# Optimization experiments

Hardware: AMD Instinct MI355X
Metric: run time of the kernel (lower is better)

## Reference

```python
import jax, jax.numpy as jnp
import numpy as np

N_HEADS = 71
HEAD_DIM = 64
ROPE_BASE = 10000.0
SCALE = 1.0 / np.sqrt(HEAD_DIM)  # 0.125


def setup_inputs() -> dict:
    key = jax.random.key(0)
    k1, k2, k3 = jax.random.split(key, 3)
    B, S, H = 1, 1024, N_HEADS * HEAD_DIM  # 4544
    F = (N_HEADS + 2) * HEAD_DIM           # 4672 fused QKV out features
    hidden_states = jax.random.normal(k1, (B, 1, S, H), dtype=jnp.float32)
    qkv_weight = jax.random.normal(k2, (H, F), dtype=jnp.float32) * 0.02
    dense_weight = jax.random.normal(k3, (H, H), dtype=jnp.float32) * 0.02
    # additive causal mask [1,1,S,S]
    causal = np.tril(np.ones((S, S), dtype=bool))
    attention_mask = jnp.asarray(np.where(causal, 0.0, -1e9).astype(np.float32))[None, None]
    return {"hidden_states": hidden_states, "qkv_weight": qkv_weight,
            "dense_weight": dense_weight, "attention_mask": attention_mask}


def _rope_tables(seq_len):
    inv_freq = 1.0 / (ROPE_BASE ** (jnp.arange(0, HEAD_DIM, 2, dtype=jnp.float32) / HEAD_DIM))
    t = jnp.arange(seq_len, dtype=jnp.float32)
    freqs = t[:, None] * inv_freq[None, :]          # [S, 32]
    emb = jnp.concatenate([freqs, freqs], axis=-1)  # [S, 64]
    return jnp.cos(emb), jnp.sin(emb)


def _rotate_half(x):
    h = HEAD_DIM // 2
    return jnp.concatenate([-x[..., h:], x[..., :h]], axis=-1)


def reference(hidden_states, qkv_weight, dense_weight, attention_mask):
    # Prefill: hidden_states [B, 1, S, H]
    B, _, S, H = hidden_states.shape
    x = hidden_states[:, 0]                                  # [B, S, H]
    qkv = jnp.einsum('bsh,hf->bsf', x, qkv_weight)           # fused QKV matmul
    qd = N_HEADS * HEAD_DIM
    # Falcon-7B MQA head split: 71 query heads, 1 shared K and V head
    q = qkv[..., :qd].reshape(B, S, N_HEADS, HEAD_DIM).transpose(0, 2, 1, 3)  # [B, nH, S, d]
    k = qkv[..., qd:qd + HEAD_DIM]                           # [B, S, d]
    v = qkv[..., qd + HEAD_DIM:]                             # [B, S, d]
    cos, sin = _rope_tables(S)                               # [S, d]
    q = q * cos + _rotate_half(q) * sin
    k = k * cos + _rotate_half(k) * sin
    scores = jnp.einsum('bhqd,bkd->bhqk', q, k) * SCALE      # [B, nH, S, S]
    scores = scores + attention_mask                         # causal mask (alibi is None for Falcon-7B)
    probs = jax.nn.softmax(scores, axis=-1)
    ctx = jnp.einsum('bhqk,bkd->bhqd', probs, v)             # [B, nH, S, d]
    merged = ctx.transpose(0, 2, 1, 3).reshape(B, S, H)      # concat heads
    out = jnp.einsum('bsh,hf->bsf', merged, dense_weight)    # selfout dense
    return out[:, None]                                      # [B, 1, S, H]
```

## Files before the change

kernel.cpp:

```cpp
#include <hip/hip_runtime.h>
#include <hip/hip_bf16.h>

#define DI __device__ __forceinline__

typedef __attribute__((ext_vector_type(8))) short bf16x8;
typedef __attribute__((ext_vector_type(4))) float f32x4;
typedef __attribute__((ext_vector_type(4))) short s16x4;

constexpr int S  = 1024;
constexpr int NH = 71;
constexpr int HD = 64;
constexpr int H  = NH * HD;
constexpr int F  = (NH + 2) * HD;
constexpr float K2 = 0.125f * 1.44269504f;

DI short f2bf(float f) {
  union { float f; unsigned u; } v; v.f = f;
  unsigned r = v.u + 0x7fffu + ((v.u >> 16) & 1u);
  return (short)(r >> 16);
}
DI unsigned cvt_pk_bf16(float lo, float hi) {
  unsigned r;
  asm("v_cvt_pk_bf16_f32 %0, %1, %2" : "=v"(r) : "v"(lo), "v"(hi));
  return r;
}
DI float redmax_g(float x) {
  float y = fmaxf(x, __int_as_float(__builtin_amdgcn_ds_swizzle(__float_as_int(x), 0x401F)));
  return fmaxf(y, __shfl_xor(y, 32));
}
DI float redsum_g(float x) {
  float y = x + __int_as_float(__builtin_amdgcn_ds_swizzle(__float_as_int(x), 0x401F));
  return y + __shfl_xor(y, 32);
}

DI void gload_lds16(const void* g, void* l) {
  __builtin_amdgcn_global_load_lds(
      (const __attribute__((address_space(1))) unsigned int*)g,
      (__attribute__((address_space(3))) unsigned int*)l, 16, 0, 0);
}

DI bf16x8 ldswz(const char* base, int row, int slot) {
  return *(const bf16x8*)(base + row * 128 + ((slot ^ (row & 7)) << 4));
}

__global__ void cast_x_kernel(const float* __restrict__ x, short* __restrict__ xb, int n4) {
  int i = blockIdx.x * blockDim.x + threadIdx.x;
  if (i >= n4) return;
  f32x4 v = ((const f32x4*)x)[i];
  s16x4 o = { f2bf(v.x), f2bf(v.y), f2bf(v.z), f2bf(v.w) };
  ((s16x4*)xb)[i] = o;
}

__global__ __launch_bounds__(256) void transpose_cast_kernel(
    const float* __restrict__ W, short* __restrict__ Wt, int K, int N) {
  __shared__ float tile[64][65];
  int n0 = blockIdx.x * 64, k0 = blockIdx.y * 64;
  int c = threadIdx.x & 63, rg = threadIdx.x >> 6;
#pragma unroll
  for (int i = 0; i < 16; ++i) {
    int r = rg * 16 + i;
    tile[r][c] = W[(size_t)(k0 + r) * N + n0 + c];
  }
  __syncthreads();
#pragma unroll
  for (int i = 0; i < 16; ++i) {
    int r = rg * 16 + i;
    Wt[(size_t)(n0 + r) * K + k0 + c] = f2bf(tile[c][r]);
  }
}

__global__ void rope_tables_kernel(float* __restrict__ ct, float* __restrict__ st) {
  int s = blockIdx.x, i = threadIdx.x;
  float invf = powf(10000.0f, -(float)i / 32.0f);
  float a = (float)s * invf;
  ct[s * 32 + i] = cosf(a);
  st[s * 32 + i] = sinf(a);
}

__global__ __launch_bounds__(256) void rope_pack_kernel(
    const float* __restrict__ qkv, const float* __restrict__ ct, const float* __restrict__ st,
    short* __restrict__ Qb, short* __restrict__ Kb, short* __restrict__ Vt) {
  int s = blockIdx.x;
  const float* row = qkv + (size_t)s * F;
  for (int c = threadIdx.x; c < F; c += 256) {
    int hh = c >> 6, d = c & 63;
    float v = row[c];
    if (hh <= NH) {
      int i = d & 31;
      float cs = ct[s * 32 + i], sn = st[s * 32 + i];
      float rot = (d < 32) ? -row[c + 32] : row[c - 32];
      short ob = f2bf(v * cs + rot * sn);
      if (hh < NH) Qb[((size_t)hh * S + s) * 64 + d] = ob;
      else         Kb[(size_t)s * 64 + d] = ob;
    } else {
      Vt[(size_t)d * S + s] = f2bf(v);
    }
  }
}

__global__ __launch_bounds__(256, 3) void gemm_bt_kernel(
    const short* __restrict__ A, const short* __restrict__ Bt, float* __restrict__ C,
    int M, int N, int K) {
  __shared__ short As[2 * 128 * 64];
  __shared__ short Bs[2 * 64 * 64];
  const int tid = threadIdx.x;
  const int lane = tid & 63;
  const int wave = tid >> 6;
  const int wr = wave >> 1, wc = wave & 1;
  const int lr = lane & 15, g = lane >> 4;

  const int nwg = gridDim.x;
  int bid = blockIdx.x;
  int wgid = ((nwg & 7) == 0) ? ((bid & 7) * (nwg >> 3) + (bid >> 3)) : bid;
  const int ntm = M >> 7;
  const int tn = wgid / ntm;
  const int tm = wgid % ntm;

  f32x4 acc[4][2] = {};

  int srowA[4], skofA[4];
#pragma unroll
  for (int iss = 0; iss < 4; ++iss) {
    int d = iss * 256 + wave * 64 + lane;
    int row = (d >> 2) & 127;
    int c = (d & 3) ^ ((row >> 1) & 3);
    srowA[iss] = row;
    skofA[iss] = ((d >> 9) << 5) + c * 8;
  }
  int srowB[2], skofB[2];
#pragma unroll
  for (int iss = 0; iss < 2; ++iss) {
    int d = iss * 256 + wave * 64 + lane;
    int row = (d >> 2) & 63;
    int c = (d & 3) ^ ((row >> 1) & 3);
    srowB[iss] = row;
    skofB[iss] = ((d >> 8) << 5) + c * 8;
  }
  int offA[2][4], offB[2][2];
#pragma unroll
  for (int im = 0; im < 4; ++im) {
    int row_a = wr * 64 + im * 16 + lr;
    int sl = (g ^ ((row_a >> 1) & 3)) << 4;
#pragma unroll
    for (int kk = 0; kk < 2; ++kk) offA[kk][im] = kk * 8192 + row_a * 64 + sl;
  }
#pragma unroll
  for (int in = 0; in < 2; ++in) {
    int row_b = wc * 32 + in * 16 + lr;
    int sl = (g ^ ((row_b >> 1) & 3)) << 4;
#pragma unroll
    for (int kk = 0; kk < 2; ++kk) offB[kk][in] = kk * 4096 + row_b * 64 + sl;
  }

  char* AsB = (char*)As;
  char* BsB = (char*)Bs;
  const size_t Abase = (size_t)tm * 128 * K;
  const size_t Bbase = (size_t)tn * 64 * K;

#define STAGE(buf, k0)                                                                  \
  {                                                                                     \
    _Pragma("unroll")                                                                   \
    for (int iss = 0; iss < 4; ++iss)                                                   \
      gload_lds16(A + Abase + (size_t)srowA[iss] * K + (k0) + skofA[iss],               \
                  AsB + (buf) * 16384 + (iss * 4 + wave) * 1024);                       \
    _Pragma("unroll")                                                                   \
    for (int iss = 0; iss < 2; ++iss)                                                   \
      gload_lds16(Bt + Bbase + (size_t)srowB[iss] * K + (k0) + skofB[iss],              \
                  BsB + (buf) * 8192 + (iss * 4 + wave) * 1024);                        \
  }

  STAGE(0, 0);
  STAGE(1, 64);
  const int KS = K >> 6;
  for (int t = 0; t < KS; ++t) {
    const int cur = t & 1;
    if (t + 1 < KS) asm volatile("s_waitcnt vmcnt(6)" ::: "memory");
    else            asm volatile("s_waitcnt vmcnt(0)" ::: "memory");
    __builtin_amdgcn_sched_barrier(0);
    __builtin_amdgcn_s_barrier();
    __builtin_amdgcn_sched_barrier(0);
    const char* Ac = AsB + cur * 16384;
    const char* Bc = BsB + cur * 8192;
    bf16x8 af[2][4], bfr[2][2];
#pragma unroll
    for (int kk = 0; kk < 2; ++kk) {
#pragma unroll
      for (int im = 0; im < 4; ++im) af[kk][im] = *(const bf16x8*)(Ac + offA[kk][im]);
#pragma unroll
      for (int in = 0; in < 2; ++in) bfr[kk][in] = *(const bf16x8*)(Bc + offB[kk][in]);
    }
#pragma unroll
    for (int kk = 0; kk < 2; ++kk)
#pragma unroll
      for (int im = 0; im < 4; ++im)
#pragma unroll
        for (int in = 0; in < 2; ++in)
          acc[im][in] = __builtin_amdgcn_mfma_f32_16x16x32_bf16(af[kk][im], bfr[kk][in], acc[im][in], 0, 0, 0);
    __builtin_amdgcn_sched_barrier(0);
    __builtin_amdgcn_s_barrier();
    __builtin_amdgcn_sched_barrier(0);
    if (t + 2 < KS) STAGE(cur, (t + 2) << 6);
  }
#undef STAGE

#pragma unroll
  for (int im = 0; im < 4; ++im) {
#pragma unroll
    for (int in = 0; in < 2; ++in) {
      int row = tm * 128 + wr * 64 + im * 16 + g * 4;
      int col = tn * 64 + wc * 32 + in * 16 + lr;
#pragma unroll
      for (int i = 0; i < 4; ++i)
        C[(size_t)(row + i) * N + col] = acc[im][in][i];
    }
  }
}

DI void attn_step(const char* Kc, const char* Vc, char* P,
                  int key0, int qrow, bf16x8 aQ0, bf16x8 aQ1,
                  f32x4* accO, float& m, float& l, int lr, int g) {
  f32x4 p[4];
#pragma unroll
  for (int nf = 0; nf < 4; ++nf) {
    int row = nf * 16 + lr;
    bf16x8 k0 = ldswz(Kc, row, g);
    bf16x8 k1 = ldswz(Kc, row, g + 4);
    f32x4 z = {};
    z = __builtin_amdgcn_mfma_f32_16x16x32_bf16(k0, aQ0, z, 0, 0, 0);
    p[nf] = __builtin_amdgcn_mfma_f32_16x16x32_bf16(k1, aQ1, z, 0, 0, 0);
  }
  float pmx = -3e30f;
#pragma unroll
  for (int nf = 0; nf < 4; ++nf)
#pragma unroll
    for (int i = 0; i < 4; ++i) {
      int key = key0 + nf * 16 + 4 * g + i;
      float sv = p[nf][i] * K2 + (key <= qrow ? 0.0f : -1e30f);
      p[nf][i] = sv;
      pmx = fmaxf(pmx, sv);
    }
  float pm = redmax_g(pmx);
  float mn = fmaxf(m, pm);
  float scl = __builtin_exp2f(m - mn);
  m = mn;
  float rsx = 0.f;
#pragma unroll
  for (int nf = 0; nf < 4; ++nf) {
    f32x4 pe;
#pragma unroll
    for (int i = 0; i < 4; ++i) {
      pe[i] = __builtin_exp2f(p[nf][i] - m);
      rsx += pe[i];
    }
    uint2 wv;
    wv.x = cvt_pk_bf16(pe[0], pe[1]);
    wv.y = cvt_pk_bf16(pe[2], pe[3]);
    *(uint2*)(P + lr * 144 + nf * 32 + g * 8) = wv;
  }
  float rs = redsum_g(rsx);
  l = l * scl + rs;
#pragma unroll
  for (int df = 0; df < 4; ++df)
#pragma unroll
    for (int i = 0; i < 4; ++i)
      accO[df][i] *= scl;
#pragma unroll
  for (int st = 0; st < 2; ++st) {
    bf16x8 bP = *(const bf16x8*)(P + lr * 144 + st * 64 + g * 16);
#pragma unroll
    for (int df = 0; df < 4; ++df) {
      bf16x8 aV = ldswz(Vc, df * 16 + lr, g + 4 * st);
      accO[df] = __builtin_amdgcn_mfma_f32_16x16x32_bf16(aV, bP, accO[df], 0, 0, 0);
    }
  }
}

__global__ __launch_bounds__(256) void attn_kernel(
    const short* __restrict__ Qb,
    const short* __restrict__ Kb,
    const short* __restrict__ Vt,
    short* __restrict__ merged) {
  __shared__ short Ks[2][4096];
  __shared__ short Vs[2][4096];
  __shared__ short Ps[4][16 * 72];
  const int lane = threadIdx.x & 63, w = threadIdx.x >> 6;
  const int lr = lane & 15, g = lane >> 4;
  const int j = blockIdx.x, head = blockIdx.y;
  const int kbmax = 15 - j;
  const int qA = j * 64 + w * 16 + lr;
  const int qB = (15 - j) * 64 + w * 16 + lr;
  char* KsB = (char*)Ks;
  char* VsB = (char*)Vs;
  char* P = (char*)Ps[w];

  int crow[2], cslot[2];
#pragma unroll
  for (int i = 0; i < 2; ++i) {
    int c = (i * 4 + w) * 64 + lane;
    crow[i] = c >> 3;
    cslot[i] = (c & 7) ^ (crow[i] & 7);
  }

  const short* qap = Qb + ((size_t)head * S + qA) * 64 + g * 8;
  bf16x8 aQA0 = *(const bf16x8*)(qap);
  bf16x8 aQA1 = *(const bf16x8*)(qap + 32);
  const short* qbp = Qb + ((size_t)head * S + qB) * 64 + g * 8;
  bf16x8 aQB0 = *(const bf16x8*)(qbp);
  bf16x8 aQB1 = *(const bf16x8*)(qbp + 32);

  f32x4 accA[4] = {}, accB[4] = {};
  float mA = -3e30f, lA = 0.f, mB = -3e30f, lB = 0.f;

#define STAGEKV(buf, key0)                                                       \
  {                                                                              \
    _Pragma("unroll")                                                            \
    for (int i = 0; i < 2; ++i) {                                                \
      gload_lds16(Kb + (size_t)((key0) + crow[i]) * 64 + cslot[i] * 8,           \
                  KsB + (buf) * 8192 + (i * 4 + w) * 1024);                      \
      gload_lds16(Vt + (size_t)crow[i] * S + (key0) + cslot[i] * 8,              \
                  VsB + (buf) * 8192 + (i * 4 + w) * 1024);                      \
    }                                                                            \
  }

  STAGEKV(0, 0);
  for (int kb = 0; kb <= kbmax; ++kb) {
    const int cur = kb & 1;
    __syncthreads();
    if (kb < kbmax) STAGEKV(cur ^ 1, (kb + 1) * 64);
    const char* Kc = KsB + cur * 8192;
    const char* Vc = VsB + cur * 8192;
    attn_step(Kc, Vc, P, kb * 64, qB, aQB0, aQB1, accB, mB, lB, lr, g);
    if (kb <= j)
      attn_step(Kc, Vc, P, kb * 64, qA, aQA0, aQA1, accA, mA, lA, lr, g);
  }
#undef STAGEKV

  float rlA = 1.0f / lA, rlB = 1.0f / lB;
#pragma unroll
  for (int df = 0; df < 4; ++df)
#pragma unroll
    for (int i = 0; i < 4; ++i) {
      int d = head * 64 + df * 16 + 4 * g + i;
      merged[(size_t)qB * H + d] = f2bf(accB[df][i] * rlB);
      merged[(size_t)qA * H + d] = f2bf(accA[df][i] * rlA);
    }
}

extern "C" void kernel_launch(void* const* d_in, const int* in_sizes, int n_in,
                              void* d_out, int out_size, void* d_ws, size_t ws_size,
                              hipStream_t stream) {
  const float* x    = (const float*)d_in[0];
  const float* wqkv = (const float*)d_in[1];
  const float* wd   = (const float*)d_in[2];
  float* out = (float*)d_out;

  char* ws = (char*)d_ws;
  size_t off = 0;
  short* Wqkvt  = (short*)(ws + off); off += (size_t)F * H * 2;
  short* Wdt    = (short*)(ws + off); off += (size_t)H * H * 2;
  short* Qb     = (short*)(ws + off); off += (size_t)NH * S * HD * 2;
  short* Kb     = (short*)(ws + off); off += (size_t)S * HD * 2;
  short* Vtb    = (short*)(ws + off); off += (size_t)HD * S * 2;
  short* merged = (short*)(ws + off); off += (size_t)S * H * 2;
  float* ct     = (float*)(ws + off); off += (size_t)S * 32 * 4;
  float* st     = (float*)(ws + off); off += (size_t)S * 32 * 4;
  short* xb     = (short*)(ws + off); off += (size_t)S * H * 2;
  float* qkv    = (float*)(ws + off); off += (size_t)S * F * 4;
  (void)ws_size; (void)in_sizes; (void)n_in; (void)out_size;

  hipLaunchKernelGGL(cast_x_kernel, dim3((S * H / 4 + 255) / 256), dim3(256), 0, stream,
                     x, xb, S * H / 4);
  hipLaunchKernelGGL(transpose_cast_kernel, dim3(F / 64, H / 64), dim3(256), 0, stream,
                     wqkv, Wqkvt, H, F);
  hipLaunchKernelGGL(transpose_cast_kernel, dim3(H / 64, H / 64), dim3(256), 0, stream,
                     wd, Wdt, H, H);
  hipLaunchKernelGGL(rope_tables_kernel, dim3(S), dim3(32), 0, stream, ct, st);
  hipLaunchKernelGGL(gemm_bt_kernel, dim3((F / 64) * (S / 128)), dim3(256), 0, stream,
                     xb, Wqkvt, qkv, S, F, H);
  hipLaunchKernelGGL(rope_pack_kernel, dim3(S), dim3(256), 0, stream,
                     qkv, ct, st, Qb, Kb, Vtb);
  hipLaunchKernelGGL(attn_kernel, dim3(8, NH), dim3(256), 0, stream,
                     Qb, Kb, Vtb, merged);
  hipLaunchKernelGGL(gemm_bt_kernel, dim3((H / 64) * (S / 128)), dim3(256), 0, stream,
                     merged, Wdt, out, S, H, H);
}
```

Measured before the change: 244.1 us.

## Replace tiled GEMM with stream-K persistent GEMM using atomic partial accumulation

Both projection GEMMs now use a persistent stream-K kernel with 256 workgroups of 512 threads and 128x128 tiles. The K-iteration space is split evenly across workgroups, and partial tiles are merged into the output with float atomicAdd. This targets wave-quantization imbalance from the ragged tile counts (73 or 71 N tiles by 8 M tiles). In exchange the outputs must be zeroed first by extra kernels, atomics add memory traffic, and the summation order becomes nondeterministic. The kernel also raises MFMA priority with setprio.

New measurement: 324.4 us. 32.9% more time.

```diff
diff --git a/kernel.cpp b/kernel.cpp
--- a/kernel.cpp
+++ b/kernel.cpp
@@ -41,6 +41,13 @@
 
 DI bf16x8 ldswz(const char* base, int row, int slot) {
   return *(const bf16x8*)(base + row * 128 + ((slot ^ (row & 7)) << 4));
+}
+
+__global__ void zero_kernel(float* __restrict__ p, int n4) {
+  int i = blockIdx.x * blockDim.x + threadIdx.x;
+  if (i >= n4) return;
+  f32x4 z = {0.f, 0.f, 0.f, 0.f};
+  ((f32x4*)p)[i] = z;
 }
 
 __global__ void cast_x_kernel(const float* __restrict__ x, short* __restrict__ xb, int n4) {
@@ -98,121 +105,128 @@
   }
 }
 
-__global__ __launch_bounds__(256, 3) void gemm_bt_kernel(
+__global__ __launch_bounds__(512, 2) void gemm_streamk_kernel(
     const short* __restrict__ A, const short* __restrict__ Bt, float* __restrict__ C,
-    int M, int N, int K) {
-  __shared__ short As[2 * 128 * 64];
-  __shared__ short Bs[2 * 64 * 64];
+    int N, int K, int U) {
+  __shared__ f32x4 smemv[4096];
+  char* smem = (char*)smemv;
   const int tid = threadIdx.x;
-  const int lane = tid & 63;
-  const int wave = tid >> 6;
-  const int wr = wave >> 1, wc = wave & 1;
+  const int lane = tid & 63, wave = tid >> 6;
+  const int wr = wave >> 2, wc = wave & 3;
   const int lr = lane & 15, g = lane >> 4;
-
-  const int nwg = gridDim.x;
-  int bid = blockIdx.x;
-  int wgid = ((nwg & 7) == 0) ? ((bid & 7) * (nwg >> 3) + (bid >> 3)) : bid;
-  const int ntm = M >> 7;
-  const int tn = wgid / ntm;
-  const int tm = wgid % ntm;
-
-  f32x4 acc[4][2] = {};
-
-  int srowA[4], skofA[4];
-#pragma unroll
-  for (int iss = 0; iss < 4; ++iss) {
-    int d = iss * 256 + wave * 64 + lane;
+  const int nk = K >> 6;
+
+  const int bid = blockIdx.x;
+  const int swz = ((bid & 7) << 5) | (bid >> 3);
+  const int q = U >> 8, r = U & 255;
+  const int start = swz * q + (swz < r ? swz : r);
+  const int end = start + q + (swz < r ? 1 : 0);
+
+  int rowS[2], kofS[2];
+#pragma unroll
+  for (int iss = 0; iss < 2; ++iss) {
+    int d = iss * 512 + tid;
     int row = (d >> 2) & 127;
     int c = (d & 3) ^ ((row >> 1) & 3);
-    srowA[iss] = row;
-    skofA[iss] = ((d >> 9) << 5) + c * 8;
-  }
-  int srowB[2], skofB[2];
-#pragma unroll
-  for (int iss = 0; iss < 2; ++iss) {
-    int d = iss * 256 + wave * 64 + lane;
-    int row = (d >> 2) & 63;
-    int c = (d & 3) ^ ((row >> 1) & 3);
-    srowB[iss] = row;
-    skofB[iss] = ((d >> 8) << 5) + c * 8;
+    rowS[iss] = row;
+    kofS[iss] = ((d >> 9) << 5) + c * 8;
   }
   int offA[2][4], offB[2][2];
 #pragma unroll
   for (int im = 0; im < 4; ++im) {
-    int row_a = wr * 64 + im * 16 + lr;
-    int sl = (g ^ ((row_a >> 1) & 3)) << 4;
-#pragma unroll
-    for (int kk = 0; kk < 2; ++kk) offA[kk][im] = kk * 8192 + row_a * 64 + sl;
+    int ra = wr * 64 + im * 16 + lr;
+    int sl = (g ^ ((ra >> 1) & 3)) << 4;
+#pragma unroll
+    for (int kk = 0; kk < 2; ++kk) offA[kk][im] = kk * 8192 + ra * 64 + sl;
   }
 #pragma unroll
   for (int in = 0; in < 2; ++in) {
-    int row_b = wc * 32 + in * 16 + lr;
-    int sl = (g ^ ((row_b >> 1) & 3)) << 4;
-#pragma unroll
-    for (int kk = 0; kk < 2; ++kk) offB[kk][in] = kk * 4096 + row_b * 64 + sl;
-  }
-
-  char* AsB = (char*)As;
-  char* BsB = (char*)Bs;
-  const size_t Abase = (size_t)tm * 128 * K;
-  const size_t Bbase = (size_t)tn * 64 * K;
-
-#define STAGE(buf, k0)                                                                  \
-  {                                                                                     \
-    _Pragma("unroll")                                                                   \
-    for (int iss = 0; iss < 4; ++iss)                                                   \
-      gload_lds16(A + Abase + (size_t)srowA[iss] * K + (k0) + skofA[iss],               \
-                  AsB + (buf) * 16384 + (iss * 4 + wave) * 1024);                       \
-    _Pragma("unroll")                                                                   \
-    for (int iss = 0; iss < 2; ++iss)                                                   \
-      gload_lds16(Bt + Bbase + (size_t)srowB[iss] * K + (k0) + skofB[iss],              \
-                  BsB + (buf) * 8192 + (iss * 4 + wave) * 1024);                        \
-  }
-
-  STAGE(0, 0);
-  STAGE(1, 64);
-  const int KS = K >> 6;
-  for (int t = 0; t < KS; ++t) {
-    const int cur = t & 1;
-    if (t + 1 < KS) asm volatile("s_waitcnt vmcnt(6)" ::: "memory");
-    else            asm volatile("s_waitcnt vmcnt(0)" ::: "memory");
-    __builtin_amdgcn_sched_barrier(0);
-    __builtin_amdgcn_s_barrier();
-    __builtin_amdgcn_sched_barrier(0);
-    const char* Ac = AsB + cur * 16384;
-    const char* Bc = BsB + cur * 8192;
-    bf16x8 af[2][4], bfr[2][2];
-#pragma unroll
-    for (int kk = 0; kk < 2; ++kk) {
-#pragma unroll
-      for (int im = 0; im < 4; ++im) af[kk][im] = *(const bf16x8*)(Ac + offA[kk][im]);
-#pragma unroll
-      for (int in = 0; in < 2; ++in) bfr[kk][in] = *(const bf16x8*)(Bc + offB[kk][in]);
-    }
-#pragma unroll
-    for (int kk = 0; kk < 2; ++kk)
-#pragma unroll
-      for (int im = 0; im < 4; ++im)
-#pragma unroll
-        for (int in = 0; in < 2; ++in)
-          acc[im][in] = __builtin_amdgcn_mfma_f32_16x16x32_bf16(af[kk][im], bfr[kk][in], acc[im][in], 0, 0, 0);
-    __builtin_amdgcn_sched_barrier(0);
-    __builtin_amdgcn_s_barrier();
-    __builtin_amdgcn_sched_barrier(0);
-    if (t + 2 < KS) STAGE(cur, (t + 2) << 6);
-  }
-#undef STAGE
-
-#pragma unroll
-  for (int im = 0; im < 4; ++im) {
-#pragma unroll
-    for (int in = 0; in < 2; ++in) {
-      int row = tm * 128 + wr * 64 + im * 16 + g * 4;
-      int col = tn * 64 + wc * 32 + in * 16 + lr;
-#pragma unroll
-      for (int i = 0; i < 4; ++i)
-        C[(size_t)(row + i) * N + col] = acc[im][in][i];
-    }
+    int rb = wc * 32 + in * 16 + lr;
+    int sl = (g ^ ((rb >> 1) & 3)) << 4;
+#pragma unroll
+    for (int kk = 0; kk < 2; ++kk) offB[kk][in] = kk * 8192 + rb * 64 + sl;
+  }
+
+  int u = start;
+  while (u < end) {
+    const int tt = u / nk;
+    const int k0 = u - tt * nk;
+    int kn = nk - k0; if (kn > end - u) kn = end - u;
+    const int tm = tt & 7, tn = tt >> 3;
+
+    const short* Ab[2]; const short* Bb[2];
+#pragma unroll
+    for (int iss = 0; iss < 2; ++iss) {
+      Ab[iss] = A + (size_t)(tm * 128 + rowS[iss]) * K + kofS[iss];
+      int bn = tn * 128 + rowS[iss]; if (bn >= N) bn = N - 1;
+      Bb[iss] = Bt + (size_t)bn * K + kofS[iss];
+    }
+
+#define SK_STAGE(buf, ks)                                                       \
+    { _Pragma("unroll")                                                         \
+      for (int iss = 0; iss < 2; ++iss) {                                       \
+        gload_lds16(Ab[iss] + (ks) * 64,                                        \
+                    smem + (buf) * 16384 + (iss * 8 + wave) * 1024);            \
+        gload_lds16(Bb[iss] + (ks) * 64,                                        \
+                    smem + 32768 + (buf) * 16384 + (iss * 8 + wave) * 1024);    \
+      } }
+
+    f32x4 acc[4][2] = {};
+    SK_STAGE(0, k0);
+    if (kn > 1) SK_STAGE(1, k0 + 1);
+    for (int t = 0; t < kn; ++t) {
+      const int cur = t & 1;
+      if (t + 1 < kn) asm volatile("s_waitcnt vmcnt(4)" ::: "memory");
+      else            asm volatile("s_waitcnt vmcnt(0)" ::: "memory");
+      __builtin_amdgcn_sched_barrier(0);
+      __builtin_amdgcn_s_barrier();
+      __builtin_amdgcn_sched_barrier(0);
+      const char* Ac = smem + cur * 16384;
+      const char* Bc = smem + 32768 + cur * 16384;
+      bf16x8 af[2][4], bfr[2][2];
+#pragma unroll
+      for (int kk = 0; kk < 2; ++kk) {
+#pragma unroll
+        for (int im = 0; im < 4; ++im) af[kk][im] = *(const bf16x8*)(Ac + offA[kk][im]);
+#pragma unroll
+        for (int in = 0; in < 2; ++in) bfr[kk][in] = *(const bf16x8*)(Bc + offB[kk][in]);
+      }
+      __builtin_amdgcn_s_setprio(1);
+#pragma unroll
+      for (int kk = 0; kk < 2; ++kk)
+#pragma unroll
+        for (int im = 0; im < 4; ++im)
+#pragma unroll
+          for (int in = 0; in < 2; ++in)
+            acc[im][in] = __builtin_amdgcn_mfma_f32_16x16x32_bf16(af[kk][im], bfr[kk][in], acc[im][in], 0, 0, 0);
+      __builtin_amdgcn_s_setprio(0);
+      __builtin_amdgcn_sched_barrier(0);
+      __builtin_amdgcn_s_barrier();
+      __builtin_amdgcn_sched_barrier(0);
+      if (t + 2 < kn) SK_STAGE(cur, k0 + t + 2);
+    }
+#undef SK_STAGE
+
+    const bool full = (k0 == 0) && (kn == nk);
+#pragma unroll
+    for (int im = 0; im < 4; ++im)
+#pragma unroll
+      for (int in = 0; in < 2; ++in) {
+        int rowc = tm * 128 + wr * 64 + im * 16 + g * 4;
+        int colc = tn * 128 + wc * 32 + in * 16 + lr;
+        if (colc < N) {
+          if (full) {
+#pragma unroll
+            for (int i = 0; i < 4; ++i)
+              C[(size_t)(rowc + i) * N + colc] = acc[im][in][i];
+          } else {
+#pragma unroll
+            for (int i = 0; i < 4; ++i)
+              atomicAdd(&C[(size_t)(rowc + i) * N + colc], acc[im][in][i]);
+          }
+        }
+      }
+    u += kn;
   }
 }
 
@@ -368,6 +382,10 @@
   float* qkv    = (float*)(ws + off); off += (size_t)S * F * 4;
   (void)ws_size; (void)in_sizes; (void)n_in; (void)out_size;
 
+  hipLaunchKernelGGL(zero_kernel, dim3((S * F / 4 + 255) / 256), dim3(256), 0, stream,
+                     qkv, S * F / 4);
+  hipLaunchKernelGGL(zero_kernel, dim3((S * H / 4 + 255) / 256), dim3(256), 0, stream,
+                     out, S * H / 4);
   hipLaunchKernelGGL(cast_x_kernel, dim3((S * H / 4 + 255) / 256), dim3(256), 0, stream,
                      x, xb, S * H / 4);
   hipLaunchKernelGGL(transpose_cast_kernel, dim3(F / 64, H / 64), dim3(256), 0, stream,
@@ -375,12 +393,12 @@
   hipLaunchKernelGGL(transpose_cast_kernel, dim3(H / 64, H / 64), dim3(256), 0, stream,
                      wd, Wdt, H, H);
   hipLaunchKernelGGL(rope_tables_kernel, dim3(S), dim3(32), 0, stream, ct, st);
-  hipLaunchKernelGGL(gemm_bt_kernel, dim3((F / 64) * (S / 128)), dim3(256), 0, stream,
-                     xb, Wqkvt, qkv, S, F, H);
+  hipLaunchKernelGGL(gemm_streamk_kernel, dim3(256), dim3(512), 0, stream,
+                     xb, Wqkvt, qkv, F, H, 296 * 71);
   hipLaunchKernelGGL(rope_pack_kernel, dim3(S), dim3(256), 0, stream,
                      qkv, ct, st, Qb, Kb, Vtb);
   hipLaunchKernelGGL(attn_kernel, dim3(8, NH), dim3(256), 0, stream,
                      Qb, Kb, Vtb, merged);
-  hipLaunchKernelGGL(gemm_bt_kernel, dim3((H / 64) * (S / 128)), dim3(256), 0, stream,
-                     merged, Wdt, out, S, H, H);
-}
+  hipLaunchKernelGGL(gemm_streamk_kernel, dim3(256), dim3(512), 0, stream,
+                     merged, Wdt, out, H, H, 288 * 71);
+}
```
